# Optimization experiments

Hardware: AMD Instinct MI355X
Metric: run time of the kernel (lower is better)

Reference implementation:

```python
import jax, jax.numpy as jnp
import numpy as np

E, TOPK, H, I = 8, 2, 2048, 5632
T = 4096


def setup_inputs() -> dict:
    key = jax.random.key(0)
    k1, k2, k3, k4 = jax.random.split(key, 4)
    hidden_states = jax.random.normal(k1, (T, H), dtype=jnp.float32)
    gate_w = jax.random.normal(k2, (E, H), dtype=jnp.float32) * (1.0 / np.sqrt(H))
    # fused gate+up projection: [E, 2*I, H]
    w13 = jax.random.normal(k3, (E, 2 * I, H), dtype=jnp.float32) * (1.0 / np.sqrt(H))
    # down projection: [E, H, I]
    w2 = jax.random.normal(k4, (E, H, I), dtype=jnp.float32) * (1.0 / np.sqrt(I))
    return {"hidden_states": hidden_states, "gate_w": gate_w, "w13": w13, "w2": w2, "top_k": TOPK}


def reference(hidden_states, gate_w, w13, w2, top_k):
    num_experts = gate_w.shape[0]
    inter = w2.shape[2]
    # router: fp32 gate logits -> softmax -> top-k -> renormalize (FusedMoE renormalize=True)
    logits = hidden_states.astype(jnp.float32) @ gate_w.T          # [T, E]
    probs = jax.nn.softmax(logits, axis=-1)
    vals, idx = jax.lax.top_k(probs, top_k)                        # [T, k]
    vals = vals / jnp.sum(vals, axis=-1, keepdims=True)
    # dense routing weight matrix [T, E] (zero outside top-k)
    dense_w = jnp.sum(jax.nn.one_hot(idx, num_experts, dtype=vals.dtype) * vals[..., None], axis=1)

    def body(acc, inputs):
        w13_e, w2_e, we = inputs                                   # [2I,H], [H,I], [T]
        gu = hidden_states @ w13_e.T                               # [T, 2I]
        g, u = gu[:, :inter], gu[:, inter:]
        h = jax.nn.silu(g) * u                                     # SwiGLU
        y = h @ w2_e.T                                             # [T, H]
        return acc + we[:, None] * y, None

    acc0 = jnp.zeros_like(hidden_states)
    out, _ = jax.lax.scan(body, acc0, (w13, w2, dense_w.T))
    return out
```

## Files before the change

### kernel.cpp

```cpp
#include <hip/hip_runtime.h>

#define T_TOK 4096
#define H_DIM 2048
#define I_DIM 5632
#define NE 8

typedef _Float16 f16;
typedef _Float16 f16x8 __attribute__((ext_vector_type(8)));
typedef float f32x4 __attribute__((ext_vector_type(4)));

#define OFF_META   0
#define OFF_BTOK   256
#define OFF_BW     (256 + 32768)
#define OFF_RE     (256 + 2 * 32768)
#define OFF_RW     (256 + 3 * 32768)
#define OFF_TP     (256 + 4 * 32768)
#define OFF_HSB    (256 + 5 * 32768)
#define OFF_WF     (OFF_HSB + (size_t)T_TOK * H_DIM * 2)

typedef const __attribute__((address_space(1))) unsigned int guint;
typedef __attribute__((address_space(3))) unsigned int luint;

__device__ __forceinline__ int swzk(int r, int bir) {
    return (bir & 15) | ((((bir >> 4) ^ r) & 7) << 4);
}

__global__ void cvt_w_kernel(const float* __restrict__ src, f16* __restrict__ dst, int n8) {
    int stride = gridDim.x * blockDim.x;
    for (int i = blockIdx.x * blockDim.x + threadIdx.x; i < n8; i += stride) {
        size_t b = (size_t)i * 8;
        float4 a = *(const float4*)(src + b);
        float4 c = *(const float4*)(src + b + 4);
        f16x8 v;
        v[0] = (f16)a.x; v[1] = (f16)a.y; v[2] = (f16)a.z; v[3] = (f16)a.w;
        v[4] = (f16)c.x; v[5] = (f16)c.y; v[6] = (f16)c.z; v[7] = (f16)c.w;
        *(f16x8*)(dst + b) = v;
    }
}

__global__ void prep_kernel(const float* __restrict__ w13, f16* __restrict__ w13f, int n8_w13,
                            int cvt13_b,
                            const float* __restrict__ hs, f16* __restrict__ hsb,
                            const float* __restrict__ gw,
                            int* __restrict__ re, float* __restrict__ rw,
                            int* __restrict__ counts) {
    int id = blockIdx.x;
    if (id < cvt13_b) {
        int stride = cvt13_b * 256;
        for (int i = id * 256 + threadIdx.x; i < n8_w13; i += stride) {
            size_t b = (size_t)i * 8;
            float4 a = *(const float4*)(w13 + b);
            float4 c = *(const float4*)(w13 + b + 4);
            f16x8 v;
            v[0] = (f16)a.x; v[1] = (f16)a.y; v[2] = (f16)a.z; v[3] = (f16)a.w;
            v[4] = (f16)c.x; v[5] = (f16)c.y; v[6] = (f16)c.z; v[7] = (f16)c.w;
            *(f16x8*)(w13f + b) = v;
        }
        return;
    }
    id -= cvt13_b;
    if (id < 1024) {
        const int n8 = T_TOK * H_DIM / 8;
        int stride = 1024 * 256;
        for (int i = id * 256 + threadIdx.x; i < n8; i += stride) {
            size_t b = (size_t)i * 8;
            float4 a = *(const float4*)(hs + b);
            float4 c = *(const float4*)(hs + b + 4);
            f16x8 v;
            v[0] = (f16)a.x; v[1] = (f16)a.y; v[2] = (f16)a.z; v[3] = (f16)a.w;
            v[4] = (f16)c.x; v[5] = (f16)c.y; v[6] = (f16)c.z; v[7] = (f16)c.w;
            *(f16x8*)(hsb + b) = v;
        }
        return;
    }
    id -= 1024;
    int lane = threadIdx.x & 63;
    int t = id * 4 + (threadIdx.x >> 6);
    float acc[NE];
#pragma unroll
    for (int e = 0; e < NE; ++e) acc[e] = 0.f;
    const float* x = hs + (size_t)t * H_DIM;
    for (int i = lane; i < H_DIM; i += 64) {
        float xv = x[i];
#pragma unroll
        for (int e = 0; e < NE; ++e) acc[e] += xv * gw[e * H_DIM + i];
    }
#pragma unroll
    for (int e = 0; e < NE; ++e)
        for (int off = 32; off > 0; off >>= 1) acc[e] += __shfl_xor(acc[e], off);
    if (lane == 0) {
        int i1 = 0; float l1 = acc[0];
#pragma unroll
        for (int e = 1; e < NE; ++e) if (acc[e] > l1) { l1 = acc[e]; i1 = e; }
        int i2 = -1; float l2 = -1e30f;
#pragma unroll
        for (int e = 0; e < NE; ++e) if (e != i1 && acc[e] > l2) { l2 = acc[e]; i2 = e; }
        float aa = __expf(l2 - l1);
        float s = 1.f / (1.f + aa);
        re[t * 2] = i1; re[t * 2 + 1] = i2;
        rw[t * 2] = s;  rw[t * 2 + 1] = aa * s;
        atomicAdd(&counts[i1], 1);
        atomicAdd(&counts[i2], 1);
    }
}

__global__ void scan_kernel(int* __restrict__ meta) {
    if (threadIdx.x == 0) {
        int s = 0;
        for (int e = 0; e < NE; ++e) { meta[8 + e] = s; meta[16 + e] = s; s += meta[e]; }
    }
}

__global__ void place_kernel(const int* __restrict__ re, const float* __restrict__ rw,
                             int* __restrict__ cursor, int* __restrict__ btok,
                             float* __restrict__ bwv, int* __restrict__ tpos) {
    int t = blockIdx.x * 256 + threadIdx.x;
    if (t >= T_TOK) return;
#pragma unroll
    for (int s = 0; s < 2; ++s) {
        int e = re[t * 2 + s];
        int p = atomicAdd(&cursor[e], 1);
        btok[p] = t;
        bwv[p] = rw[t * 2 + s];
        tpos[t * 2 + s] = p;
    }
}

__device__ __forceinline__ void decode_panel(int id, int npx, int e_arg,
                                             int& e, int& bx, int& by) {
    if (e_arg >= 0) { e = e_arg; bx = id >> 5; by = id & 31; return; }
    int sg  = id >> 8;
    int rem = id & 255;
    by = rem >> 3;
    int P = sg * 8 + (rem & 7);
    e = P / npx; bx = P % npx;
}

__global__ __launch_bounds__(256, 4) void gemm1_kernel(
    const f16* __restrict__ w13f, const f16* __restrict__ hsb, f16* __restrict__ hb,
    const int* __restrict__ counts, const int* __restrict__ offs,
    const int* __restrict__ btok,
    const float* __restrict__ w2src, f16* __restrict__ w2dst, int cvt_n8, int cvt_blocks,
    int e_arg, int global_h)
{
    if ((int)blockIdx.x < cvt_blocks) {
        int stride = cvt_blocks * 256;
        for (int i = blockIdx.x * 256 + threadIdx.x; i < cvt_n8; i += stride) {
            size_t b = (size_t)i * 8;
            float4 a = *(const float4*)(w2src + b);
            float4 c = *(const float4*)(w2src + b + 4);
            f16x8 v;
            v[0] = (f16)a.x; v[1] = (f16)a.y; v[2] = (f16)a.z; v[3] = (f16)a.w;
            v[4] = (f16)c.x; v[5] = (f16)c.y; v[6] = (f16)c.z; v[7] = (f16)c.w;
            *(f16x8*)(w2dst + b) = v;
        }
        return;
    }
    int e, bx, by;
    decode_panel((int)blockIdx.x - cvt_blocks, 88, e_arg, e, bx, by);
    const int n_e = counts[e];
    if (by * 128 >= n_e) return;
    const int boff = offs[e];
    const f16* We = (e_arg >= 0) ? w13f : (w13f + (size_t)e * (2 * I_DIM) * H_DIM);

    const int tid = threadIdx.x;
    const int lane = tid & 63;
    const int wid = tid >> 6;
    const int wm = wid >> 1, wn = wid & 1;
    const int l15 = lane & 15;

    __shared__ f16 As[128 * 64];
    __shared__ f16 Bs[128 * 64];

    const f16* gA[4]; const f16* gB[4]; int dstc[4];
#pragma unroll
    for (int i = 0; i < 4; ++i) {
        int c = i * 256 + tid;
        int r = c >> 3;
        dstc[i] = c * 16;
        int slot = ((c & 7) ^ (r & 7)) * 8;
        int idx = by * 128 + r;
        idx = idx < n_e ? idx : n_e - 1;
        gA[i] = hsb + (size_t)btok[boff + idx] * H_DIM + slot;
        int wrow = (r < 64) ? (bx * 64 + r) : (I_DIM + bx * 64 + (r - 64));
        gB[i] = We + (size_t)wrow * H_DIM + slot;
    }

    f32x4 ag[4][2], au[4][2];
#pragma unroll
    for (int m = 0; m < 4; ++m)
#pragma unroll
        for (int n = 0; n < 2; ++n) { ag[m][n] = (f32x4)0.f; au[m][n] = (f32x4)0.f; }

    const int NT = H_DIM / 64;

#pragma unroll 1
    for (int kt = 0; kt < NT; ++kt) {
        __syncthreads();
        const int k0 = kt * 64;
#pragma unroll
        for (int i = 0; i < 4; ++i) {
            __builtin_amdgcn_global_load_lds((guint*)(gA[i] + k0), (luint*)((char*)As + dstc[i]), 16, 0, 0);
            __builtin_amdgcn_global_load_lds((guint*)(gB[i] + k0), (luint*)((char*)Bs + dstc[i]), 16, 0, 0);
        }
        __syncthreads();
#pragma unroll
        for (int kh = 0; kh < 2; ++kh) {
            const int kb = kh * 64 + (lane >> 4) * 16;
            f16x8 a[4], bg[2], bu[2];
#pragma unroll
            for (int m = 0; m < 4; ++m) {
                int r = wm * 64 + m * 16 + l15;
                a[m] = *(const f16x8*)((const char*)As + r * 128 + swzk(r, kb));
            }
#pragma unroll
            for (int n = 0; n < 2; ++n) {
                int rg = wn * 32 + n * 16 + l15;
                bg[n] = *(const f16x8*)((const char*)Bs + rg * 128 + swzk(rg, kb));
                int ru = 64 + rg;
                bu[n] = *(const f16x8*)((const char*)Bs + ru * 128 + swzk(ru, kb));
            }
#pragma unroll
            for (int m = 0; m < 4; ++m)
#pragma unroll
                for (int n = 0; n < 2; ++n) {
                    ag[m][n] = __builtin_amdgcn_mfma_f32_16x16x32_f16(a[m], bg[n], ag[m][n], 0, 0, 0);
                    au[m][n] = __builtin_amdgcn_mfma_f32_16x16x32_f16(a[m], bu[n], au[m][n], 0, 0, 0);
                }
        }
    }

    const int hbase = (global_h ? boff : 0) + by * 128;
#pragma unroll
    for (int m = 0; m < 4; ++m) {
        int rl0 = wm * 64 + m * 16 + ((lane >> 4) << 2);
#pragma unroll
        for (int r = 0; r < 4; ++r) {
            int rl = rl0 + r;
            if (by * 128 + rl < n_e) {
#pragma unroll
                for (int n = 0; n < 2; ++n) {
                    float g = ag[m][n][r];
                    float u = au[m][n][r];
                    float h = g / (1.f + __expf(-g)) * u;
                    hb[(size_t)(hbase + rl) * I_DIM + bx * 64 + wn * 32 + n * 16 + l15] = (f16)h;
                }
            }
        }
    }
}

__global__ __launch_bounds__(256, 4) void gemm2_kernel(
    const f16* __restrict__ w2f, const f16* __restrict__ hb, float* __restrict__ y,
    const int* __restrict__ counts, const int* __restrict__ offs,
    const int* __restrict__ btok, int e_arg, int global_h)
{
    int e, bx, by;
    decode_panel(blockIdx.x, 16, e_arg, e, bx, by);
    const int n_e = counts[e];
    if (by * 128 >= n_e) return;
    const int boff = offs[e];
    const f16* We = (e_arg >= 0) ? w2f : (w2f + (size_t)e * H_DIM * I_DIM);

    const int tid = threadIdx.x;
    const int lane = tid & 63;
    const int wid = tid >> 6;
    const int wm = wid >> 1, wn = wid & 1;
    const int l15 = lane & 15;

    __shared__ f16 As[128 * 64];
    __shared__ f16 Bs[128 * 64];

    const int hb0 = global_h ? boff : 0;
    const f16* gA[4]; const f16* gB[4]; int dstc[4];
#pragma unroll
    for (int i = 0; i < 4; ++i) {
        int c = i * 256 + tid;
        int r = c >> 3;
        dstc[i] = c * 16;
        int slot = ((c & 7) ^ (r & 7)) * 8;
        int idx = by * 128 + r;
        idx = idx < n_e ? idx : n_e - 1;
        gA[i] = hb + (size_t)(hb0 + idx) * I_DIM + slot;
        gB[i] = We + (size_t)(bx * 128 + r) * I_DIM + slot;
    }

    f32x4 acc[4][4];
#pragma unroll
    for (int m = 0; m < 4; ++m)
#pragma unroll
        for (int n = 0; n < 4; ++n) acc[m][n] = (f32x4)0.f;

    const int NT = I_DIM / 64;

#pragma unroll 1
    for (int kt = 0; kt < NT; ++kt) {
        __syncthreads();
        const int k0 = kt * 64;
#pragma unroll
        for (int i = 0; i < 4; ++i) {
            __builtin_amdgcn_global_load_lds((guint*)(gA[i] + k0), (luint*)((char*)As + dstc[i]), 16, 0, 0);
            __builtin_amdgcn_global_load_lds((guint*)(gB[i] + k0), (luint*)((char*)Bs + dstc[i]), 16, 0, 0);
        }
        __syncthreads();
#pragma unroll
        for (int kh = 0; kh < 2; ++kh) {
            const int kb = kh * 64 + (lane >> 4) * 16;
            f16x8 a[4], b[4];
#pragma unroll
            for (int m = 0; m < 4; ++m) {
                int r = wm * 64 + m * 16 + l15;
                a[m] = *(const f16x8*)((const char*)As + r * 128 + swzk(r, kb));
            }
#pragma unroll
            for (int n = 0; n < 4; ++n) {
                int r = wn * 64 + n * 16 + l15;
                b[n] = *(const f16x8*)((const char*)Bs + r * 128 + swzk(r, kb));
            }
#pragma unroll
            for (int m = 0; m < 4; ++m)
#pragma unroll
                for (int n = 0; n < 4; ++n)
                    acc[m][n] = __builtin_amdgcn_mfma_f32_16x16x32_f16(a[m], b[n], acc[m][n], 0, 0, 0);
        }
    }

#pragma unroll
    for (int m = 0; m < 4; ++m) {
        int rl0 = wm * 64 + m * 16 + ((lane >> 4) << 2);
#pragma unroll
        for (int r = 0; r < 4; ++r) {
            int rl = rl0 + r;
            if (by * 128 + rl < n_e) {
                int p = boff + by * 128 + rl;
#pragma unroll
                for (int n = 0; n < 4; ++n)
                    y[(size_t)p * H_DIM + bx * 128 + wn * 64 + n * 16 + l15] = acc[m][n][r];
            }
        }
    }
}

__global__ void reduce_kernel(const float* __restrict__ y, const int* __restrict__ tpos,
                              const float* __restrict__ bwv, float* __restrict__ out) {
    int t = blockIdx.x;
    int p0 = tpos[t * 2], p1 = tpos[t * 2 + 1];
    float w0 = bwv[p0], w1 = bwv[p1];
    const float4* y0 = (const float4*)(y + (size_t)p0 * H_DIM);
    const float4* y1 = (const float4*)(y + (size_t)p1 * H_DIM);
    float4* o = (float4*)(out + (size_t)t * H_DIM);
    for (int i = threadIdx.x; i < H_DIM / 4; i += 256) {
        float4 a = y0[i], b = y1[i];
        float4 r;
        r.x = w0 * a.x + w1 * b.x;
        r.y = w0 * a.y + w1 * b.y;
        r.z = w0 * a.z + w1 * b.z;
        r.w = w0 * a.w + w1 * b.w;
        o[i] = r;
    }
}

extern "C" void kernel_launch(void* const* d_in, const int* in_sizes, int n_in,
                              void* d_out, int out_size, void* d_ws, size_t ws_size,
                              hipStream_t stream) {
    const float* hs  = (const float*)d_in[0];
    const float* gw  = (const float*)d_in[1];
    const float* w13 = (const float*)d_in[2];
    const float* w2  = (const float*)d_in[3];
    float* out = (float*)d_out;

    char* ws = (char*)d_ws;
    int*   meta = (int*)(ws + OFF_META);
    int*   btok = (int*)(ws + OFF_BTOK);
    float* bwv  = (float*)(ws + OFF_BW);
    int*   re   = (int*)(ws + OFF_RE);
    float* rw   = (float*)(ws + OFF_RW);
    int*   tpos = (int*)(ws + OFF_TP);
    f16*   hsb  = (f16*)(ws + OFF_HSB);

    hipMemsetAsync(meta, 0, 256, stream);

    const size_t w13_elems = (size_t)NE * 2 * I_DIM * H_DIM;
    const size_t w2_elems  = (size_t)NE * H_DIM * I_DIM;

    size_t o_w13f = OFF_WF;
    size_t o_w2f  = o_w13f + w13_elems * 2;
    size_t o_hb   = o_w2f + w2_elems * 2;
    size_t o_y    = o_hb + (size_t)2 * T_TOK * I_DIM * 2;
    size_t need_full = o_y + (size_t)2 * T_TOK * H_DIM * 4;

    size_t f_w13 = OFF_WF;
    size_t f_w2  = f_w13 + (size_t)2 * I_DIM * H_DIM * 2;
    size_t f_hb  = f_w2 + (size_t)H_DIM * I_DIM * 2;
    size_t f_y   = f_hb + (size_t)T_TOK * I_DIM * 2;

    if (ws_size >= need_full) {
        f16* w13f = (f16*)(ws + o_w13f);
        f16* w2f  = (f16*)(ws + o_w2f);
        f16* hb   = (f16*)(ws + o_hb);
        float* y  = (float*)(ws + o_y);
        prep_kernel<<<3072 + 1024 + 1024, 256, 0, stream>>>(
            w13, w13f, (int)(w13_elems / 8), 3072, hs, hsb, gw, re, rw, meta);
        scan_kernel<<<1, 64, 0, stream>>>(meta);
        place_kernel<<<T_TOK / 256, 256, 0, stream>>>(re, rw, meta + 16, btok, bwv, tpos);
        gemm1_kernel<<<2048 + 704 * 32, 256, 0, stream>>>(
            w13f, hsb, hb, meta, meta + 8, btok,
            w2, w2f, (int)(w2_elems / 8), 2048, -1, 1);
        gemm2_kernel<<<128 * 32, 256, 0, stream>>>(w2f, hb, y, meta, meta + 8, btok, -1, 1);
        reduce_kernel<<<T_TOK, 256, 0, stream>>>(y, tpos, bwv, out);
    } else {
        f16* w13f = (f16*)(ws + f_w13);
        f16* w2f  = (f16*)(ws + f_w2);
        f16* hb   = (f16*)(ws + f_hb);
        float* y  = (float*)(ws + f_y);
        prep_kernel<<<1024 + 1024, 256, 0, stream>>>(
            w13, (f16*)nullptr, 0, 0, hs, hsb, gw, re, rw, meta);
        scan_kernel<<<1, 64, 0, stream>>>(meta);
        place_kernel<<<T_TOK / 256, 256, 0, stream>>>(re, rw, meta + 16, btok, bwv, tpos);
        const size_t w13_slice = (size_t)2 * I_DIM * H_DIM;
        const size_t w2_slice  = (size_t)H_DIM * I_DIM;
        for (int e = 0; e < NE; ++e) {
            cvt_w_kernel<<<2048, 256, 0, stream>>>(w13 + e * w13_slice, w13f, (int)(w13_slice / 8));
            gemm1_kernel<<<2048 + 88 * 32, 256, 0, stream>>>(
                w13f, hsb, hb, meta, meta + 8, btok,
                w2 + e * w2_slice, w2f, (int)(w2_slice / 8), 2048, e, 0);
            gemm2_kernel<<<16 * 32, 256, 0, stream>>>(w2f, hb, y, meta, meta + 8, btok, e, 0);
        }
        reduce_kernel<<<T_TOK, 256, 0, stream>>>(y, tpos, bwv, out);
    }
}
```

Measured before the change: 1.136 ms.

## Split gemm1 into two expert halves overlapping w13 conversion, widen gemm2 tiles

The w13 fp32→fp16 conversion is split in two. The prep kernel converts only experts 0-3, and the first gemm1 launch (experts 0-3) converts experts 4-7 in its spare blocks. The second gemm1 launch (experts 4-7) converts w2 in the same way, so weight conversion overlaps with the GEMM work. gemm2 moves to 512-thread blocks computing 128x256 output tiles, which halves the number of A-tile reloads of the intermediate activations. The risks are an extra kernel launch, lower occupancy from the larger LDS footprint and 512 threads, and fewer blocks in gemm2.

```diff
diff --git a/kernel.cpp b/kernel.cpp
--- a/kernel.cpp
+++ b/kernel.cpp
@@ -126,38 +126,38 @@
     }
 }
 
-__device__ __forceinline__ void decode_panel(int id, int npx, int e_arg,
+__device__ __forceinline__ void decode_panel(int id, int npx, int e_arg, int e_base,
                                              int& e, int& bx, int& by) {
     if (e_arg >= 0) { e = e_arg; bx = id >> 5; by = id & 31; return; }
     int sg  = id >> 8;
     int rem = id & 255;
     by = rem >> 3;
     int P = sg * 8 + (rem & 7);
-    e = P / npx; bx = P % npx;
+    e = e_base + P / npx; bx = P % npx;
 }
 
 __global__ __launch_bounds__(256, 4) void gemm1_kernel(
     const f16* __restrict__ w13f, const f16* __restrict__ hsb, f16* __restrict__ hb,
     const int* __restrict__ counts, const int* __restrict__ offs,
     const int* __restrict__ btok,
-    const float* __restrict__ w2src, f16* __restrict__ w2dst, int cvt_n8, int cvt_blocks,
-    int e_arg, int global_h)
+    const float* __restrict__ cvt_src, f16* __restrict__ cvt_dst, int cvt_n8, int cvt_blocks,
+    int e_arg, int e_base, int global_h)
 {
     if ((int)blockIdx.x < cvt_blocks) {
         int stride = cvt_blocks * 256;
         for (int i = blockIdx.x * 256 + threadIdx.x; i < cvt_n8; i += stride) {
             size_t b = (size_t)i * 8;
-            float4 a = *(const float4*)(w2src + b);
-            float4 c = *(const float4*)(w2src + b + 4);
+            float4 a = *(const float4*)(cvt_src + b);
+            float4 c = *(const float4*)(cvt_src + b + 4);
             f16x8 v;
             v[0] = (f16)a.x; v[1] = (f16)a.y; v[2] = (f16)a.z; v[3] = (f16)a.w;
             v[4] = (f16)c.x; v[5] = (f16)c.y; v[6] = (f16)c.z; v[7] = (f16)c.w;
-            *(f16x8*)(w2dst + b) = v;
+            *(f16x8*)(cvt_dst + b) = v;
         }
         return;
     }
     int e, bx, by;
-    decode_panel((int)blockIdx.x - cvt_blocks, 88, e_arg, e, bx, by);
+    decode_panel((int)blockIdx.x - cvt_blocks, 88, e_arg, e_base, e, bx, by);
     const int n_e = counts[e];
     if (by * 128 >= n_e) return;
     const int boff = offs[e];
@@ -250,13 +250,13 @@
     }
 }
 
-__global__ __launch_bounds__(256, 4) void gemm2_kernel(
+__global__ __launch_bounds__(512, 4) void gemm2_kernel(
     const f16* __restrict__ w2f, const f16* __restrict__ hb, float* __restrict__ y,
     const int* __restrict__ counts, const int* __restrict__ offs,
     const int* __restrict__ btok, int e_arg, int global_h)
 {
     int e, bx, by;
-    decode_panel(blockIdx.x, 16, e_arg, e, bx, by);
+    decode_panel(blockIdx.x, 8, e_arg, 0, e, bx, by);
     const int n_e = counts[e];
     if (by * 128 >= n_e) return;
     const int boff = offs[e];
@@ -265,24 +265,33 @@
     const int tid = threadIdx.x;
     const int lane = tid & 63;
     const int wid = tid >> 6;
-    const int wm = wid >> 1, wn = wid & 1;
+    const int wm = wid >> 2;
+    const int wn = wid & 3;
     const int l15 = lane & 15;
 
     __shared__ f16 As[128 * 64];
-    __shared__ f16 Bs[128 * 64];
+    __shared__ f16 Bs[256 * 64];
 
     const int hb0 = global_h ? boff : 0;
-    const f16* gA[4]; const f16* gB[4]; int dstc[4];
-#pragma unroll
-    for (int i = 0; i < 4; ++i) {
-        int c = i * 256 + tid;
+    const f16* gA[2]; int dA[2];
+#pragma unroll
+    for (int i = 0; i < 2; ++i) {
+        int c = i * 512 + tid;
         int r = c >> 3;
-        dstc[i] = c * 16;
+        dA[i] = c * 16;
         int slot = ((c & 7) ^ (r & 7)) * 8;
         int idx = by * 128 + r;
         idx = idx < n_e ? idx : n_e - 1;
         gA[i] = hb + (size_t)(hb0 + idx) * I_DIM + slot;
-        gB[i] = We + (size_t)(bx * 128 + r) * I_DIM + slot;
+    }
+    const f16* gB[4]; int dB[4];
+#pragma unroll
+    for (int j = 0; j < 4; ++j) {
+        int c = j * 512 + tid;
+        int r = c >> 3;
+        dB[j] = c * 16;
+        int slot = ((c & 7) ^ (r & 7)) * 8;
+        gB[j] = We + (size_t)(bx * 256 + r) * I_DIM + slot;
     }
 
     f32x4 acc[4][4];
@@ -298,10 +307,11 @@
         __syncthreads();
         const int k0 = kt * 64;
 #pragma unroll
-        for (int i = 0; i < 4; ++i) {
-            __builtin_amdgcn_global_load_lds((guint*)(gA[i] + k0), (luint*)((char*)As + dstc[i]), 16, 0, 0);
-            __builtin_amdgcn_global_load_lds((guint*)(gB[i] + k0), (luint*)((char*)Bs + dstc[i]), 16, 0, 0);
-        }
+        for (int i = 0; i < 2; ++i)
+            __builtin_amdgcn_global_load_lds((guint*)(gA[i] + k0), (luint*)((char*)As + dA[i]), 16, 0, 0);
+#pragma unroll
+        for (int j = 0; j < 4; ++j)
+            __builtin_amdgcn_global_load_lds((guint*)(gB[j] + k0), (luint*)((char*)Bs + dB[j]), 16, 0, 0);
         __syncthreads();
 #pragma unroll
         for (int kh = 0; kh < 2; ++kh) {
@@ -335,7 +345,7 @@
                 int p = boff + by * 128 + rl;
 #pragma unroll
                 for (int n = 0; n < 4; ++n)
-                    y[(size_t)p * H_DIM + bx * 128 + wn * 64 + n * 16 + l15] = acc[m][n][r];
+                    y[(size_t)p * H_DIM + bx * 256 + wn * 64 + n * 16 + l15] = acc[m][n][r];
             }
         }
     }
@@ -381,6 +391,7 @@
     hipMemsetAsync(meta, 0, 256, stream);
 
     const size_t w13_elems = (size_t)NE * 2 * I_DIM * H_DIM;
+    const size_t w13_half  = w13_elems / 2;
     const size_t w2_elems  = (size_t)NE * H_DIM * I_DIM;
 
     size_t o_w13f = OFF_WF;
@@ -400,13 +411,16 @@
         f16* hb   = (f16*)(ws + o_hb);
         float* y  = (float*)(ws + o_y);
         prep_kernel<<<3072 + 1024 + 1024, 256, 0, stream>>>(
-            w13, w13f, (int)(w13_elems / 8), 3072, hs, hsb, gw, re, rw, meta);
+            w13, w13f, (int)(w13_half / 8), 3072, hs, hsb, gw, re, rw, meta);
         scan_kernel<<<1, 64, 0, stream>>>(meta);
         place_kernel<<<T_TOK / 256, 256, 0, stream>>>(re, rw, meta + 16, btok, bwv, tpos);
-        gemm1_kernel<<<2048 + 704 * 32, 256, 0, stream>>>(
+        gemm1_kernel<<<2048 + 352 * 32, 256, 0, stream>>>(
             w13f, hsb, hb, meta, meta + 8, btok,
-            w2, w2f, (int)(w2_elems / 8), 2048, -1, 1);
-        gemm2_kernel<<<128 * 32, 256, 0, stream>>>(w2f, hb, y, meta, meta + 8, btok, -1, 1);
+            w13 + w13_half, (f16*)(ws + o_w13f) + w13_half, (int)(w13_half / 8), 2048, -1, 0, 1);
+        gemm1_kernel<<<2048 + 352 * 32, 256, 0, stream>>>(
+            w13f, hsb, hb, meta, meta + 8, btok,
+            w2, w2f, (int)(w2_elems / 8), 2048, -1, 4, 1);
+        gemm2_kernel<<<64 * 32, 512, 0, stream>>>(w2f, hb, y, meta, meta + 8, btok, -1, 1);
         reduce_kernel<<<T_TOK, 256, 0, stream>>>(y, tpos, bwv, out);
     } else {
         f16* w13f = (f16*)(ws + f_w13);
@@ -423,8 +437,8 @@
             cvt_w_kernel<<<2048, 256, 0, stream>>>(w13 + e * w13_slice, w13f, (int)(w13_slice / 8));
             gemm1_kernel<<<2048 + 88 * 32, 256, 0, stream>>>(
                 w13f, hsb, hb, meta, meta + 8, btok,
-                w2 + e * w2_slice, w2f, (int)(w2_slice / 8), 2048, e, 0);
-            gemm2_kernel<<<16 * 32, 256, 0, stream>>>(w2f, hb, y, meta, meta + 8, btok, e, 0);
+                w2 + e * w2_slice, w2f, (int)(w2_slice / 8), 2048, e, 0, 0);
+            gemm2_kernel<<<8 * 32, 512, 0, stream>>>(w2f, hb, y, meta, meta + 8, btok, e, 0);
         }
         reduce_kernel<<<T_TOK, 256, 0, stream>>>(y, tpos, bwv, out);
     }
```

Measured after the change: 1.185 ms. 4.3% more time.
